# Kernel tuning notes

Hardware: AMD Instinct MI355X
Metric: run time of the kernel (lower is better)

The kernel has to match this reference:

```python
import jax, jax.numpy as jnp
import numpy as np

B, S, D, E, K = 4, 4096, 4096, 64, 8

def setup_inputs() -> dict:
    key = jax.random.key(0)
    kx, kw = jax.random.split(key)
    x = jax.random.normal(kx, (B, S, D), dtype=jnp.float32)
    W = jax.random.normal(kw, (D, E), dtype=jnp.float32) * (1.0 / np.sqrt(D))
    b = jnp.zeros((E,), dtype=jnp.float32)
    return {"x": x, "W": W, "b": b, "k": K}

def reference(x, W, b, k):
    # s: sigmoid router scores [B, S, E]
    s = jax.nn.sigmoid(jnp.einsum('bsd,de->bse', x, W) + b)
    # per-token top-k over experts
    g_i, indices = jax.lax.top_k(s, k)  # [B, S, k]
    # scatter-normalize-gather collapses to: normalize top-k gates by their sum
    # (zeros everywhere else contribute nothing to the sum)
    g_scores = g_i / jnp.sum(g_i, axis=-1, keepdims=True)
    return (g_scores, indices, s)
```

## Files before the change

### kernel.cpp

```cpp
#include <hip/hip_runtime.h>
#include <cmath>

#define NTOK 16384
#define DDIM 4096
#define NEXP 64
#define TOPK 8
#define TPB   256
#define NKS   8
#define KSL   (DDIM / NKS)
#define BK    32
#define NSTEP (KSL / BK)
#define EPS_GAP 6e-5f

typedef __attribute__((ext_vector_type(8))) short short8;
typedef __attribute__((ext_vector_type(4))) float f32x4;

__device__ __forceinline__ void gload16(const void* g, void* l) {
    __builtin_amdgcn_global_load_lds(
        (const __attribute__((address_space(1))) unsigned int*)g,
        (__attribute__((address_space(3))) unsigned int*)l, 16, 0, 0);
}

#define CVT1(f, hOut, lOut, j) do {                                          \
    unsigned _u = __builtin_bit_cast(unsigned, (float)(f));                  \
    float _hf = __builtin_bit_cast(float, _u & 0xFFFF0000u);                 \
    hOut[j] = (short)(_u >> 16);                                             \
    lOut[j] = (short)(__builtin_bit_cast(unsigned, (float)((f) - _hf)) >> 16);\
} while (0)
#define CONV8(vA, vB, hOut, lOut) do {                       \
    CVT1(vA.x, hOut, lOut, 0); CVT1(vA.y, hOut, lOut, 1);    \
    CVT1(vA.z, hOut, lOut, 2); CVT1(vA.w, hOut, lOut, 3);    \
    CVT1(vB.x, hOut, lOut, 4); CVT1(vB.y, hOut, lOut, 5);    \
    CVT1(vB.z, hOut, lOut, 6); CVT1(vB.w, hOut, lOut, 7);    \
} while (0)

__global__ __launch_bounds__(256) void prep_w(const float* __restrict__ W,
                                              unsigned char* __restrict__ blob,
                                              int* __restrict__ cnts)
{
    __shared__ float tile[32][65];
    const int c = blockIdx.x;
    const int t = threadIdx.x;
    if (c == 0 && t < 4) cnts[t] = 0;
    {
        const int r = t >> 3, q = t & 7;
        float4 v0 = *reinterpret_cast<const float4*>(
            &W[(size_t)(c * 32 + r) * NEXP + q * 8]);
        float4 v1 = *reinterpret_cast<const float4*>(
            &W[(size_t)(c * 32 + r) * NEXP + q * 8 + 4]);
        tile[r][q * 8 + 0] = v0.x; tile[r][q * 8 + 1] = v0.y;
        tile[r][q * 8 + 2] = v0.z; tile[r][q * 8 + 3] = v0.w;
        tile[r][q * 8 + 4] = v1.x; tile[r][q * 8 + 5] = v1.y;
        tile[r][q * 8 + 6] = v1.z; tile[r][q * 8 + 7] = v1.w;
    }
    __syncthreads();
    {
        const int el   = t & 15;
        const int kgrp = (t >> 4) & 3;
        const int n    = t >> 6;
        short8 hv, lv;
#pragma unroll
        for (int j = 0; j < 8; ++j) {
            float f = tile[kgrp * 8 + j][n * 16 + el];
            CVT1(f, hv, lv, j);
        }
        unsigned char* base = blob + (size_t)c * 8192 + n * 2048 +
                              (kgrp * 16 + el) * 16;
        *reinterpret_cast<short8*>(base)        = hv;
        *reinterpret_cast<short8*>(base + 1024) = lv;
    }
}

__global__ __launch_bounds__(512, 4) void bulk_kernel(
    const float* __restrict__ x, const unsigned char* __restrict__ blob,
    float* __restrict__ part)
{
    __shared__ __align__(16) unsigned char smem[81920];

    const int tid  = threadIdx.x;
    const int l    = tid & 63;
    const int w    = tid >> 6;
    const int tokg = blockIdx.x >> 3;
    const int ks   = blockIdx.x & 7;
    const int tok0 = tokg * TPB;

#define DECLA(q) const float* aSrc##q = x +                                   \
    (size_t)(tok0 + q * 64 + (tid >> 3)) * DDIM + ks * KSL +                  \
    ((((tid & 7) ^ ((tid >> 3) & 7))) << 2);
    DECLA(0) DECLA(1) DECLA(2) DECLA(3)
#undef DECLA
    const unsigned char* bSrc = blob + (size_t)(ks * NSTEP) * 8192 + tid * 16;

#define STAGE(buf, c) do {                                                    \
    unsigned char* _a = smem + (buf) * 32768;                                 \
    gload16(aSrc0 + (size_t)(c) * BK, _a + 0 * 8192 + tid * 16);              \
    gload16(aSrc1 + (size_t)(c) * BK, _a + 1 * 8192 + tid * 16);              \
    gload16(aSrc2 + (size_t)(c) * BK, _a + 2 * 8192 + tid * 16);              \
    gload16(aSrc3 + (size_t)(c) * BK, _a + 3 * 8192 + tid * 16);              \
    gload16(bSrc + (size_t)(c) * 8192, smem + 65536 + (buf) * 8192 + tid * 16);\
} while (0)

    const int mt   = l & 15;
    const int kgrp = l >> 4;
    const int sw   = mt & 7;
    const int row0 = w * 32 + mt;
    const int row1 = row0 + 16;
    const int aoff00 = row0 * 128 + (((kgrp * 2    ) ^ sw) << 4);
    const int aoff01 = row0 * 128 + (((kgrp * 2 + 1) ^ sw) << 4);
    const int aoff10 = row1 * 128 + (((kgrp * 2    ) ^ sw) << 4);
    const int aoff11 = row1 * 128 + (((kgrp * 2 + 1) ^ sw) << 4);

    f32x4 acc00 = (f32x4){0.f,0.f,0.f,0.f}, acc01 = acc00, acc02 = acc00, acc03 = acc00;
    f32x4 acc10 = acc00, acc11 = acc00, acc12 = acc00, acc13 = acc00;

#define MFMA3(accv, AH, AL, BH, BL) do {                                      \
    accv = __builtin_amdgcn_mfma_f32_16x16x32_bf16(AH, BH, accv, 0, 0, 0);    \
    accv = __builtin_amdgcn_mfma_f32_16x16x32_bf16(AH, BL, accv, 0, 0, 0);    \
    accv = __builtin_amdgcn_mfma_f32_16x16x32_bf16(AL, BH, accv, 0, 0, 0);    \
} while (0)

#define COMPUTE(buf) do {                                                     \
    const unsigned char* _a  = smem + (buf) * 32768;                          \
    const unsigned char* _bb = smem + 65536 + (buf) * 8192;                   \
    float4 A0 = *reinterpret_cast<const float4*>(_a + aoff00);                \
    float4 A1 = *reinterpret_cast<const float4*>(_a + aoff01);                \
    float4 A2 = *reinterpret_cast<const float4*>(_a + aoff10);                \
    float4 A3 = *reinterpret_cast<const float4*>(_a + aoff11);                \
    short8 ah0, al0, ah1, al1;                                                \
    CONV8(A0, A1, ah0, al0);                                                  \
    CONV8(A2, A3, ah1, al1);                                                  \
    {                                                                         \
        short8 bh = *reinterpret_cast<const short8*>(_bb + 0 * 2048 + l * 16);\
        short8 bl = *reinterpret_cast<const short8*>(_bb + 0 * 2048 + 1024 + l * 16);\
        MFMA3(acc00, ah0, al0, bh, bl); MFMA3(acc10, ah1, al1, bh, bl);       \
    }                                                                         \
    {                                                                         \
        short8 bh = *reinterpret_cast<const short8*>(_bb + 1 * 2048 + l * 16);\
        short8 bl = *reinterpret_cast<const short8*>(_bb + 1 * 2048 + 1024 + l * 16);\
        MFMA3(acc01, ah0, al0, bh, bl); MFMA3(acc11, ah1, al1, bh, bl);       \
    }                                                                         \
    {                                                                         \
        short8 bh = *reinterpret_cast<const short8*>(_bb + 2 * 2048 + l * 16);\
        short8 bl = *reinterpret_cast<const short8*>(_bb + 2 * 2048 + 1024 + l * 16);\
        MFMA3(acc02, ah0, al0, bh, bl); MFMA3(acc12, ah1, al1, bh, bl);       \
    }                                                                         \
    {                                                                         \
        short8 bh = *reinterpret_cast<const short8*>(_bb + 3 * 2048 + l * 16);\
        short8 bl = *reinterpret_cast<const short8*>(_bb + 3 * 2048 + 1024 + l * 16);\
        MFMA3(acc03, ah0, al0, bh, bl); MFMA3(acc13, ah1, al1, bh, bl);       \
    }                                                                         \
} while (0)

    STAGE(0, 0);
    STAGE(1, 1);
    for (int c = 0; c < NSTEP; ++c) {
        if (c < NSTEP - 1) {
            asm volatile("s_waitcnt vmcnt(5)\n\ts_barrier" ::: "memory");
        } else {
            asm volatile("s_waitcnt vmcnt(0)\n\ts_barrier" ::: "memory");
        }
        COMPUTE(c & 1);
        __builtin_amdgcn_s_barrier();
        if (c + 2 < NSTEP) STAGE(c & 1, c + 2);
    }

#define WRPART(tf, n, accv) do {                                              \
    _Pragma("unroll")                                                         \
    for (int r = 0; r < 4; ++r)                                               \
        part[((size_t)ks * NTOK + tok0 + w * 32 + tf * 16 + kgrp * 4 + r)     \
             * NEXP + n * 16 + mt] = accv[r];                                 \
} while (0)
    WRPART(0, 0, acc00); WRPART(0, 1, acc01); WRPART(0, 2, acc02); WRPART(0, 3, acc03);
    WRPART(1, 0, acc10); WRPART(1, 1, acc11); WRPART(1, 2, acc12); WRPART(1, 3, acc13);
#undef WRPART
#undef STAGE
#undef COMPUTE
#undef MFMA3
}

__global__ __launch_bounds__(256) void combine_kernel(
    const float* __restrict__ part, const float* __restrict__ b,
    float* __restrict__ g_out, float* __restrict__ i_out,
    float* __restrict__ s_out,
    int* __restrict__ flag_cnt, int* __restrict__ flag_list, int cap)
{
    __shared__ float ls[64 * 68];
    const int tid  = threadIdx.x;
    const int tok0 = blockIdx.x * 64;
    const int t    = tid >> 2;
    const int e16  = (tid & 3) * 16;

#pragma unroll
    for (int g = 0; g < 4; ++g) {
        const int e = e16 + g * 4;
        const size_t base = ((size_t)(tok0 + t)) * NEXP + e;
        float4 a = *reinterpret_cast<const float4*>(&part[base]);
#pragma unroll
        for (int s = 1; s < NKS; ++s) {
            float4 v = *reinterpret_cast<const float4*>(
                &part[(size_t)s * NTOK * NEXP + base]);
            a.x += v.x; a.y += v.y; a.z += v.z; a.w += v.w;
        }
        float4 bv = *reinterpret_cast<const float4*>(&b[e]);
        a.x += bv.x; a.y += bv.y; a.z += bv.z; a.w += bv.w;
        *reinterpret_cast<float4*>(&ls[t * 68 + e]) = a;
        float4 sv;
        sv.x = 1.0f / (1.0f + __expf(-a.x));
        sv.y = 1.0f / (1.0f + __expf(-a.y));
        sv.z = 1.0f / (1.0f + __expf(-a.z));
        sv.w = 1.0f / (1.0f + __expf(-a.w));
        *reinterpret_cast<float4*>(&s_out[(size_t)(tok0 + t) * NEXP + e]) = sv;
    }
    __syncthreads();

    if (tid < 64) {
        const int tk = tid;
        float val[10];
        int   idx[10];
#pragma unroll
        for (int j = 0; j < 10; ++j) { val[j] = -1e30f; idx[j] = 0; }
        for (int e = 0; e < NEXP; ++e) {
            float v = ls[tk * 68 + e];
            int  ei = e;
#pragma unroll
            for (int j = 0; j < 10; ++j) {
                if (v > val[j]) {
                    float tv = val[j]; val[j] = v; v = tv;
                    int   ti = idx[j]; idx[j] = ei; ei = ti;
                }
            }
        }
        bool flag = false;
#pragma unroll
        for (int j = 0; j < 9; ++j) flag |= (val[j] - val[j + 1]) < EPS_GAP;

        float gg[TOPK], gsum = 0.0f;
#pragma unroll
        for (int j = 0; j < TOPK; ++j) {
            gg[j] = 1.0f / (1.0f + __expf(-val[j]));
            gsum += gg[j];
        }
        const float inv = 1.0f / gsum;
        const int tglob = tok0 + tk;
#pragma unroll
        for (int j = 0; j < TOPK; ++j) {
            g_out[(size_t)tglob * TOPK + j] = gg[j] * inv;
            i_out[(size_t)tglob * TOPK + j] = (float)idx[j];
        }
        if (flag) {
            int p = atomicAdd(flag_cnt, 1);
            if (p < cap) flag_list[p] = tglob;
        }
    }
}

__global__ __launch_bounds__(256) void refine64(
    const float* __restrict__ x, const float* __restrict__ W,
    const float* __restrict__ b, float* __restrict__ g_out,
    float* __restrict__ i_out, float* __restrict__ s_out,
    const int* __restrict__ flag_cnt, const int* __restrict__ flag_list,
    int flag_cap)
{
    __shared__ float  xs2[DDIM];
    __shared__ double red[4][NEXP];
    __shared__ double sc[NEXP];

    const int tid = threadIdx.x;
    int count = *flag_cnt;
    if (count > flag_cap) count = flag_cap;

    for (int it = blockIdx.x; it < count; it += gridDim.x) {
        const int tok = flag_list[it];
        __syncthreads();
#pragma unroll
        for (int q = 0; q < 4; ++q) {
            int fi = tid + 256 * q;
            *reinterpret_cast<float4*>(&xs2[fi * 4]) =
                *reinterpret_cast<const float4*>(&x[(size_t)tok * DDIM + fi * 4]);
        }
        __syncthreads();

        const int e    = tid & 63;
        const int pt   = tid >> 6;
        const int dbase = pt * (DDIM / 4);
        double a = 0.0;
        for (int d = 0; d < DDIM / 4; ++d) {
            a = fma((double)xs2[dbase + d],
                    (double)W[(size_t)(dbase + d) * NEXP + e], a);
        }
        red[pt][e] = a;
        __syncthreads();

        if (tid < NEXP) {
            double z = ((red[0][tid] + red[1][tid]) +
                        (red[2][tid] + red[3][tid])) + (double)b[tid];
            double s = 1.0 / (1.0 + exp(-z));
            sc[tid] = s;
            s_out[(size_t)tok * NEXP + tid] = (float)s;
        }
        __syncthreads();

        if (tid == 0) {
            double val[TOPK];
            int    idx[TOPK];
#pragma unroll
            for (int j = 0; j < TOPK; ++j) { val[j] = -1e30; idx[j] = 0; }
            for (int e2 = 0; e2 < NEXP; ++e2) {
                double v = sc[e2];
                int   ei = e2;
#pragma unroll
                for (int j = 0; j < TOPK; ++j) {
                    if (v > val[j]) {
                        double tv = val[j]; val[j] = v; v = tv;
                        int    ti = idx[j]; idx[j] = ei; ei = ti;
                    }
                }
            }
            double gsum = 0.0;
#pragma unroll
            for (int j = 0; j < TOPK; ++j) gsum += val[j];
            const double inv = 1.0 / gsum;
#pragma unroll
            for (int j = 0; j < TOPK; ++j) {
                g_out[(size_t)tok * TOPK + j] = (float)(val[j] * inv);
                i_out[(size_t)tok * TOPK + j] = (float)idx[j];
            }
        }
        __syncthreads();
    }
}

extern "C" void kernel_launch(void* const* d_in, const int* in_sizes, int n_in,
                              void* d_out, int out_size, void* d_ws, size_t ws_size,
                              hipStream_t stream)
{
    (void)in_sizes; (void)n_in; (void)out_size;
    const float* x = (const float*)d_in[0];
    const float* W = (const float*)d_in[1];
    const float* b = (const float*)d_in[2];

    float* g_out = (float*)d_out;
    float* i_out = g_out + (size_t)NTOK * TOPK;
    float* s_out = i_out + (size_t)NTOK * TOPK;

    const size_t OFF_LIST = 1024;
    const size_t OFF_BLOB = 131072;
    const size_t OFF_PART = OFF_BLOB + 128u * 8192u;
    const size_t WS_NEED  = OFF_PART + (size_t)NKS * NTOK * NEXP * 4;
    if (ws_size < WS_NEED) return;

    char* ws = (char*)d_ws;
    int* cnt  = (int*)ws;
    int* list = (int*)(ws + OFF_LIST);
    unsigned char* blob = (unsigned char*)(ws + OFF_BLOB);
    float* part = (float*)(ws + OFF_PART);
    int cap = NTOK;

    prep_w<<<128, 256, 0, stream>>>(W, blob, cnt);
    bulk_kernel<<<(NTOK / TPB) * NKS, 512, 0, stream>>>(x, blob, part);
    combine_kernel<<<NTOK / 64, 256, 0, stream>>>(part, b, g_out, i_out, s_out,
                                                  cnt, list, cap);
    refine64<<<256, 256, 0, stream>>>(x, W, b, g_out, i_out, s_out,
                                      cnt, list, cap);
}
```

Baseline: 158.6 us.

## Fuse split-K combine and top-k into bulk kernel via last-block counter

Removes the separate combine kernel. Each bulk block atomically increments a per-token-group counter, and the last of the eight K-slice blocks to finish reduces the partial sums, applies the bias and sigmoid, and runs top-k for its 256 tokens. This saves one kernel launch and lets the reduction overlap with other blocks' GEMM work. In exchange it adds threadfences and an atomic, and the tail work is serialized in a single block per group with only 256 of 512 threads doing top-k. The refine launch is also reduced to 64 blocks.

```diff
diff --git a/kernel.cpp b/kernel.cpp
--- a/kernel.cpp
+++ b/kernel.cpp
@@ -36,12 +36,14 @@
 
 __global__ __launch_bounds__(256) void prep_w(const float* __restrict__ W,
                                               unsigned char* __restrict__ blob,
-                                              int* __restrict__ cnts)
+                                              int* __restrict__ cnts,
+                                              int* __restrict__ tokgc)
 {
     __shared__ float tile[32][65];
     const int c = blockIdx.x;
     const int t = threadIdx.x;
     if (c == 0 && t < 4) cnts[t] = 0;
+    if (c == 1 && t < 64) tokgc[t] = 0;
     {
         const int r = t >> 3, q = t & 7;
         float4 v0 = *reinterpret_cast<const float4*>(
@@ -73,7 +75,11 @@
 
 __global__ __launch_bounds__(512, 4) void bulk_kernel(
     const float* __restrict__ x, const unsigned char* __restrict__ blob,
-    float* __restrict__ part)
+    const float* __restrict__ b, float* __restrict__ part,
+    float* __restrict__ g_out, float* __restrict__ i_out,
+    float* __restrict__ s_out,
+    int* __restrict__ tokgc,
+    int* __restrict__ flag_cnt, int* __restrict__ flag_list, int cap)
 {
     __shared__ __align__(16) unsigned char smem[81920];
 
@@ -176,51 +182,52 @@
 #undef STAGE
 #undef COMPUTE
 #undef MFMA3
-}
-
-__global__ __launch_bounds__(256) void combine_kernel(
-    const float* __restrict__ part, const float* __restrict__ b,
-    float* __restrict__ g_out, float* __restrict__ i_out,
-    float* __restrict__ s_out,
-    int* __restrict__ flag_cnt, int* __restrict__ flag_list, int cap)
-{
-    __shared__ float ls[64 * 68];
-    const int tid  = threadIdx.x;
-    const int tok0 = blockIdx.x * 64;
-    const int t    = tid >> 2;
-    const int e16  = (tid & 3) * 16;
-
-#pragma unroll
-    for (int g = 0; g < 4; ++g) {
-        const int e = e16 + g * 4;
-        const size_t base = ((size_t)(tok0 + t)) * NEXP + e;
-        float4 a = *reinterpret_cast<const float4*>(&part[base]);
-#pragma unroll
-        for (int s = 1; s < NKS; ++s) {
-            float4 v = *reinterpret_cast<const float4*>(
-                &part[(size_t)s * NTOK * NEXP + base]);
-            a.x += v.x; a.y += v.y; a.z += v.z; a.w += v.w;
-        }
-        float4 bv = *reinterpret_cast<const float4*>(&b[e]);
-        a.x += bv.x; a.y += bv.y; a.z += bv.z; a.w += bv.w;
-        *reinterpret_cast<float4*>(&ls[t * 68 + e]) = a;
-        float4 sv;
-        sv.x = 1.0f / (1.0f + __expf(-a.x));
-        sv.y = 1.0f / (1.0f + __expf(-a.y));
-        sv.z = 1.0f / (1.0f + __expf(-a.z));
-        sv.w = 1.0f / (1.0f + __expf(-a.w));
-        *reinterpret_cast<float4*>(&s_out[(size_t)(tok0 + t) * NEXP + e]) = sv;
-    }
+
+    __threadfence();
     __syncthreads();
-
-    if (tid < 64) {
-        const int tk = tid;
+    int* lastP = (int*)(smem + 81916);
+    if (tid == 0)
+        *lastP = (atomicAdd(&tokgc[tokg], 1) == NKS - 1) ? 1 : 0;
+    __syncthreads();
+    if (!*lastP) return;
+    __threadfence();
+
+    float* ls = (float*)smem;
+    {
+        const int t   = tid >> 1;
+        const int eh2 = (tid & 1) * 32;
+#pragma unroll
+        for (int g = 0; g < 8; ++g) {
+            const int e = eh2 + g * 4;
+            const size_t base = ((size_t)(tok0 + t)) * NEXP + e;
+            float4 a = *reinterpret_cast<const float4*>(&part[base]);
+#pragma unroll
+            for (int s = 1; s < NKS; ++s) {
+                float4 v = *reinterpret_cast<const float4*>(
+                    &part[(size_t)s * NTOK * NEXP + base]);
+                a.x += v.x; a.y += v.y; a.z += v.z; a.w += v.w;
+            }
+            float4 bv = *reinterpret_cast<const float4*>(&b[e]);
+            a.x += bv.x; a.y += bv.y; a.z += bv.z; a.w += bv.w;
+            *reinterpret_cast<float4*>(&ls[t * 68 + e]) = a;
+            float4 sv;
+            sv.x = 1.0f / (1.0f + __expf(-a.x));
+            sv.y = 1.0f / (1.0f + __expf(-a.y));
+            sv.z = 1.0f / (1.0f + __expf(-a.z));
+            sv.w = 1.0f / (1.0f + __expf(-a.w));
+            *reinterpret_cast<float4*>(&s_out[base]) = sv;
+        }
+    }
+    __syncthreads();
+
+    if (tid < TPB) {
+        const int t = tid;
         float val[10];
         int   idx[10];
 #pragma unroll
         for (int j = 0; j < 10; ++j) { val[j] = -1e30f; idx[j] = 0; }
         for (int e = 0; e < NEXP; ++e) {
-            float v = ls[tk * 68 + e];
+            float v = ls[t * 68 + e];
             int  ei = e;
 #pragma unroll
             for (int j = 0; j < 10; ++j) {
@@ -241,7 +248,7 @@
             gsum += gg[j];
         }
         const float inv = 1.0f / gsum;
-        const int tglob = tok0 + tk;
+        const int tglob = tok0 + t;
 #pragma unroll
         for (int j = 0; j < TOPK; ++j) {
             g_out[(size_t)tglob * TOPK + j] = gg[j] * inv;
@@ -343,6 +350,7 @@
     float* i_out = g_out + (size_t)NTOK * TOPK;
     float* s_out = i_out + (size_t)NTOK * TOPK;
 
+    const size_t OFF_TGC  = 256;
     const size_t OFF_LIST = 1024;
     const size_t OFF_BLOB = 131072;
     const size_t OFF_PART = OFF_BLOB + 128u * 8192u;
@@ -350,16 +358,16 @@
     if (ws_size < WS_NEED) return;
 
     char* ws = (char*)d_ws;
-    int* cnt  = (int*)ws;
-    int* list = (int*)(ws + OFF_LIST);
+    int* cnt   = (int*)ws;
+    int* tokgc = (int*)(ws + OFF_TGC);
+    int* list  = (int*)(ws + OFF_LIST);
     unsigned char* blob = (unsigned char*)(ws + OFF_BLOB);
     float* part = (float*)(ws + OFF_PART);
     int cap = NTOK;
 
-    prep_w<<<128, 256, 0, stream>>>(W, blob, cnt);
-    bulk_kernel<<<(NTOK / TPB) * NKS, 512, 0, stream>>>(x, blob, part);
-    combine_kernel<<<NTOK / 64, 256, 0, stream>>>(part, b, g_out, i_out, s_out,
-                                                  cnt, list, cap);
-    refine64<<<256, 256, 0, stream>>>(x, W, b, g_out, i_out, s_out,
-                                      cnt, list, cap);
-}
+    prep_w<<<128, 256, 0, stream>>>(W, blob, cnt, tokgc);
+    bulk_kernel<<<(NTOK / TPB) * NKS, 512, 0, stream>>>(
+        x, blob, b, part, g_out, i_out, s_out, tokgc, cnt, list, cap);
+    refine64<<<64, 256, 0, stream>>>(x, W, b, g_out, i_out, s_out,
+                                     cnt, list, cap);
+}
```

Result: slower. 419.1 us (+164.3%).
